# Optimization experiments

Measured on AMD Instinct MI355X. Metric: run time of the kernel, lower is better.

Reference implementation:

```python
import jax, jax.numpy as jnp
import numpy as np

N, E = 50000, 800000
IN_CH, INTER, H1, H2 = 256, 32, 8, 8
C2 = IN_CH // H2  # 32
NEG_SLOPE = 0.2


def setup_inputs() -> dict:
    key = jax.random.key(0)
    ks = jax.random.split(key, 10)
    x = jax.random.normal(ks[0], (N, IN_CH), dtype=jnp.float32)
    edge_index = jax.random.randint(ks[1], (2, E), 0, N, dtype=jnp.int32)
    s = 0.05
    W1 = jax.random.normal(ks[2], (H1 * INTER, IN_CH), dtype=jnp.float32) * s
    att_src1 = jax.random.normal(ks[3], (1, H1, INTER), dtype=jnp.float32) * s
    att_dst1 = jax.random.normal(ks[4], (1, H1, INTER), dtype=jnp.float32) * s
    b1 = jnp.zeros((H1 * INTER,), dtype=jnp.float32)
    W2 = jax.random.normal(ks[5], (H2 * C2, H1 * INTER), dtype=jnp.float32) * s
    att_src2 = jax.random.normal(ks[6], (1, H2, C2), dtype=jnp.float32) * s
    att_dst2 = jax.random.normal(ks[7], (1, H2, C2), dtype=jnp.float32) * s
    b2 = jnp.zeros((H2 * C2,), dtype=jnp.float32)
    return {"x": x, "edge_index": edge_index,
            "W1": W1, "att_src1": att_src1, "att_dst1": att_dst1, "b1": b1,
            "W2": W2, "att_src2": att_src2, "att_dst2": att_dst2, "b2": b2}


def gat_conv(x, edge_index, W, att_src, att_dst, bias, H, C):
    # PyG GATConv (shared lin for src/dst, add_self_loops=False, concat=True)
    n = x.shape[0]
    src, dst = edge_index[0], edge_index[1]
    xw = (x @ W.T).reshape(n, H, C)                     # [N,H,C]
    a_src = jnp.sum(xw * att_src, axis=-1)              # [N,H]
    a_dst = jnp.sum(xw * att_dst, axis=-1)              # [N,H]
    e = a_src[src] + a_dst[dst]                         # [E,H]
    e = jnp.where(e >= 0, e, NEG_SLOPE * e)             # LeakyReLU(0.2)
    # segment softmax over edges grouped by destination node
    m = jax.ops.segment_max(e, dst, num_segments=n)     # [N,H]
    ex = jnp.exp(e - m[dst])
    denom = jax.ops.segment_sum(ex, dst, num_segments=n)
    alpha = ex / (denom[dst] + 1e-16)                   # [E,H]
    # weighted scatter-aggregate of source messages
    msg = xw[src] * alpha[:, :, None]                   # [E,H,C]
    out = jax.ops.segment_sum(msg, dst, num_segments=n) # [N,H,C]
    return out.reshape(n, H * C) + bias


def reference(x, edge_index, W1, att_src1, att_dst1, b1, W2, att_src2, att_dst2, b2):
    h = gat_conv(x, edge_index, W1, att_src1, att_dst1, b1, H1, INTER)
    h = jax.nn.gelu(h, approximate=False)  # F.gelu default is exact
    h = gat_conv(h, edge_index, W2, att_src2, att_dst2, b2, H2, C2)
    return h[-1]  # eval-path super node
```

## Files before the change

### kernel.cpp

```cpp
#include <hip/hip_runtime.h>
#include <math.h>

#define N_NODES 50000
#define N_EDGES 800000
#define TGT     (N_NODES - 1)
#define C2MAX   256
#define KCAP    258
#define ELMAX   256
#define ROWS    (ELMAX + 1)
#define PBLK    8
#define SCANBLK 1024
#define BMWORDS 1568

struct WS {
  int* cnt;
  int* cnt2;
  int* fin_k;
  int* e2src;
  int* g_uniq;
  int* g_slot;
  int* g_misc;
  int* l1src;
  float* W1T4;
  float* W2T4;
  float* g_xw2;
  float* g_as2;
  float* g_ad2;
  float* g_as1;
  float* g_ad1;
  float* g_xw1;
};
__host__ __device__ inline WS carve(char* ws) {
  WS w; int* p = (int*)ws;
  w.cnt = p;    p += 16;
  w.cnt2 = p;   p += 272;
  w.fin_k = p;  p += 272;
  w.e2src = p;  p += C2MAX;
  w.g_uniq = p; p += 272;
  w.g_slot = p; p += C2MAX;
  w.g_misc = p; p += 16;
  w.l1src = p;  p += KCAP * ELMAX;
  float* f = (float*)p;
  w.W1T4 = f;   f += 65536;
  w.W2T4 = f;   f += 65536;
  w.g_xw2 = f;  f += KCAP * 256;
  w.g_as2 = f;  f += KCAP * 8;
  w.g_ad2 = f;  f += KCAP * 8;
  w.g_as1 = f;  f += KCAP * ROWS * 8;
  w.g_ad1 = f;  f += KCAP * ROWS * 8;
  w.g_xw1 = f;
  return w;
}

__global__ __launch_bounds__(256) void k_scan2(const int* __restrict__ eidx,
    const float* __restrict__ W1, const float* __restrict__ W2, char* ws) {
  WS w = carve(ws);
  int t = threadIdx.x;
  __shared__ float lds[64][65];
  if (blockIdx.x < 32) {
    int m  = blockIdx.x >> 4;
    int ti = (blockIdx.x >> 2) & 3, tj = blockIdx.x & 3;
    const float* src = m ? W2 : W1;
    float*       dst = m ? w.W2T4 : w.W1T4;
    int r0 = t >> 6, cc = t & 63;
    float tmp[16];
#pragma unroll
    for (int p = 0; p < 16; ++p)
      tmp[p] = src[(ti * 64 + p * 4 + r0) * 256 + tj * 64 + cc];
#pragma unroll
    for (int p = 0; p < 16; ++p)
      lds[p * 4 + r0][cc] = tmp[p];
    __syncthreads();
    int c40 = t >> 6, o = t & 63;
#pragma unroll
    for (int p2 = 0; p2 < 4; ++p2) {
      int c4l = p2 * 4 + c40;
      float4 v = make_float4(lds[o][4 * c4l + 0], lds[o][4 * c4l + 1],
                             lds[o][4 * c4l + 2], lds[o][4 * c4l + 3]);
      ((float4*)dst)[(tj * 16 + c4l) * 256 + ti * 64 + o] = v;
    }
  }
  int tid = blockIdx.x * 256 + t;
  int nthreads = gridDim.x * 256;
  const int* esrc = eidx;
  const int4* edst4 = (const int4*)(eidx + N_EDGES);
  for (int i = tid; i < N_EDGES / 4; i += nthreads) {
    int4 d = edst4[i];
    int dv[4] = {d.x, d.y, d.z, d.w};
#pragma unroll
    for (int j = 0; j < 4; ++j)
      if (dv[j] == TGT) {
        int p = atomicAdd(&w.cnt[0], 1);
        if (p < C2MAX) w.e2src[p] = esrc[4 * i + j];
      }
  }
}

__global__ __launch_bounds__(256) void k_scan1(const int* __restrict__ eidx, char* ws) {
  WS w = carve(ws);
  int t = threadIdx.x;
  __shared__ int s_e[C2MAX], s_scan[256], s_uniq[KCAP], s_slot[C2MAX], s_kv[2];
  __shared__ unsigned s_bm[BMWORDS];
  int c2 = min(w.cnt[0], C2MAX);
  if (t < c2) s_e[t] = w.e2src[t];
  __syncthreads();
  int firstIdx = t;
  if (t < c2) {
    int s = s_e[t];
    for (int q = 0; q < t; ++q) if (s_e[q] == s) { firstIdx = q; break; }
  }
  s_scan[t] = (t < c2 && firstIdx == t) ? 1 : 0;
  __syncthreads();
  for (int off = 1; off < 256; off <<= 1) {
    int add = (t >= off) ? s_scan[t - off] : 0;
    __syncthreads();
    s_scan[t] += add;
    __syncthreads();
  }
  if (t < c2 && firstIdx == t) s_uniq[s_scan[t] - 1] = s_e[t];
  __syncthreads();
  if (t < c2) s_slot[t] = s_scan[firstIdx] - 1;
  if (t == 0) {
    int K1 = (c2 > 0) ? s_scan[255] : 0;
    int kd = -1;
    for (int i = 0; i < K1; ++i) if (s_uniq[i] == TGT) { kd = i; break; }
    if (kd < 0) { s_uniq[K1] = TGT; kd = K1; K1++; }
    s_kv[0] = K1; s_kv[1] = kd;
  }
  for (int i = t; i < BMWORDS; i += 256) s_bm[i] = 0u;
  __syncthreads();
  int K1 = s_kv[0];
  for (int i = t; i < K1; i += 256) {
    int u = s_uniq[i];
    atomicOr(&s_bm[u >> 5], 1u << (u & 31));
  }
  if (blockIdx.x == 0) {
    for (int i = t; i < K1; i += 256) w.g_uniq[i] = s_uniq[i];
    if (t < c2) w.g_slot[t] = s_slot[t];
    if (t == 0) { w.g_misc[0] = K1; w.g_misc[1] = s_kv[1]; }
  }
  __syncthreads();
  int tid = blockIdx.x * 256 + t;
  int nthreads = gridDim.x * 256;
  const int* esrc = eidx;
  const int4* edst4 = (const int4*)(eidx + N_EDGES);
  for (int i = tid; i < N_EDGES / 4; i += nthreads) {
    int4 d = edst4[i];
    int dv[4] = {d.x, d.y, d.z, d.w};
#pragma unroll
    for (int j = 0; j < 4; ++j) {
      int u = dv[j];
      if ((s_bm[u >> 5] >> (u & 31)) & 1u) {
        int k = 0;
        for (int q = 0; q < K1; ++q) if (s_uniq[q] == u) { k = q; break; }
        int p = atomicAdd(&w.cnt2[k], 1);
        if (p < ELMAX) w.l1src[k * ELMAX + p] = esrc[4 * i + j];
      }
    }
  }
}

__global__ __launch_bounds__(256) void k_fused(const float* __restrict__ x,
    const float* __restrict__ aS1, const float* __restrict__ aD1,
    const float* __restrict__ b1, const float* __restrict__ aS2,
    const float* __restrict__ aD2, const float* __restrict__ b2,
    float* __restrict__ out, char* ws) {
  WS w = carve(ws);
  int K1 = w.g_misc[0];
  int k = blockIdx.x;
  if (k >= K1) return;
  int t = threadIdx.x;
  int ne = min(w.cnt2[k], ELMAX);
  int items = ne + 1;
  int myNode = w.g_uniq[k];
  __shared__ __align__(16) float s_xsT[4 * 256];
  __shared__ float s_redS[4 * 256], s_redD[4 * 256];
  __shared__ float s_as[ROWS * 8];
  __shared__ float s_p[ELMAX * 8];
  __shared__ float s_den[8];
  __shared__ __align__(16) float s_h1[256];
  __shared__ int   s_sl[C2MAX];
  __shared__ int   s_win;
  const float4* W1v = (const float4*)w.W1T4;
  const float4* W2v = (const float4*)w.W2T4;
  const float4* xsT4 = (const float4*)s_xsT;

  for (int b = blockIdx.y; b * 4 < items; b += PBLK) {
    int base = b * 4;
    int na = min(4, items - base);
    int nd[4];
#pragma unroll
    for (int i = 0; i < 4; ++i) {
      int it = base + i;
      nd[i] = (it < ne) ? w.l1src[k * ELMAX + it] : myNode;
    }
#pragma unroll
    for (int i = 0; i < 4; ++i)
      s_xsT[t * 4 + i] = x[(size_t)nd[i] * 256 + t];
    __syncthreads();
    float a0 = 0.f, a1 = 0.f, a2 = 0.f, a3 = 0.f;
    for (int cc = 0; cc < 64; cc += 8) {
      float4 wreg[8];
#pragma unroll
      for (int j = 0; j < 8; ++j)
        wreg[j] = W1v[(size_t)(cc + j) * 256 + t];
#pragma unroll
      for (int j = 0; j < 8; ++j) {
        float4 wv = wreg[j];
        int c4 = cc + j;
        float4 x0 = xsT4[4 * c4 + 0];
        float4 x1 = xsT4[4 * c4 + 1];
        float4 x2 = xsT4[4 * c4 + 2];
        float4 x3 = xsT4[4 * c4 + 3];
        a0 = fmaf(wv.x, x0.x, a0); a0 = fmaf(wv.y, x1.x, a0); a0 = fmaf(wv.z, x2.x, a0); a0 = fmaf(wv.w, x3.x, a0);
        a1 = fmaf(wv.x, x0.y, a1); a1 = fmaf(wv.y, x1.y, a1); a1 = fmaf(wv.z, x2.y, a1); a1 = fmaf(wv.w, x3.y, a1);
        a2 = fmaf(wv.x, x0.z, a2); a2 = fmaf(wv.y, x1.z, a2); a2 = fmaf(wv.z, x2.z, a2); a2 = fmaf(wv.w, x3.z, a2);
        a3 = fmaf(wv.x, x0.w, a3); a3 = fmaf(wv.y, x1.w, a3); a3 = fmaf(wv.z, x2.w, a3); a3 = fmaf(wv.w, x3.w, a3);
      }
    }
    float accs[4] = {a0, a1, a2, a3};
    for (int i = 0; i < na; ++i) {
      int row = k * ROWS + base + i;
      w.g_xw1[(size_t)row * 256 + t] = accs[i];
      s_redS[i * 256 + t] = accs[i] * aS1[t];
      s_redD[i * 256 + t] = accs[i] * aD1[t];
    }
    __syncthreads();
    if (t < 32) {
      int i = t >> 3, h = t & 7;
      if (i < na) {
        float s = 0.f, dd = 0.f;
        for (int q = 0; q < 32; ++q) {
          s  += s_redS[i * 256 + h * 32 + q];
          dd += s_redD[i * 256 + h * 32 + q];
        }
        int row = k * ROWS + base + i;
        w.g_as1[row * 8 + h] = s;
        w.g_ad1[row * 8 + h] = dd;
      }
    }
    __syncthreads();
  }

  __syncthreads();
  if (t == 0) {
    __threadfence();
    int old = __hip_atomic_fetch_add(&w.fin_k[k], 1, __ATOMIC_ACQ_REL, __HIP_MEMORY_SCOPE_AGENT);
    s_win = (old == PBLK - 1);
  }
  __syncthreads();
  if (!s_win) return;
  __threadfence();

  for (int i = t; i < items * 8; i += 256) s_as[i] = w.g_as1[(size_t)(k * ROWS) * 8 + i];
  __syncthreads();
  if (t < 8) {
    int h = t;
    float adst = w.g_ad1[(size_t)(k * ROWS + ne) * 8 + h];
    float m = -INFINITY;
    for (int j = 0; j < ne; ++j) {
      float e = s_as[j * 8 + h] + adst;
      e = (e >= 0.f) ? e : 0.2f * e;
      m = fmaxf(m, e);
    }
    float den = 0.f;
    for (int j = 0; j < ne; ++j) {
      float e = s_as[j * 8 + h] + adst;
      e = (e >= 0.f) ? e : 0.2f * e;
      float p = expf(e - m);
      s_p[j * 8 + h] = p;
      den += p;
    }
    s_den[h] = den + 1e-16f;
  }
  __syncthreads();
  int h = t >> 5;
  float acc = 0.f;
  const float* xwb = w.g_xw1 + (size_t)(k * ROWS) * 256 + t;
  for (int j0 = 0; j0 < ne; j0 += 8) {
    float tmp[8];
#pragma unroll
    for (int j = 0; j < 8; ++j)
      tmp[j] = (j0 + j < ne) ? xwb[(size_t)(j0 + j) * 256] : 0.f;
#pragma unroll
    for (int j = 0; j < 8; ++j)
      if (j0 + j < ne) acc = fmaf(s_p[(j0 + j) * 8 + h], tmp[j], acc);
  }
  float o = (ne > 0) ? acc / s_den[h] : 0.f;
  o += b1[t];
  s_h1[t] = 0.5f * o * (1.f + erff(o * 0.70710678118654752440f));
  __syncthreads();
  float a2s = 0.f;
  const float4* h1v = (const float4*)s_h1;
  for (int cc = 0; cc < 64; cc += 8) {
    float4 wreg[8];
#pragma unroll
    for (int j = 0; j < 8; ++j)
      wreg[j] = W2v[(size_t)(cc + j) * 256 + t];
#pragma unroll
    for (int j = 0; j < 8; ++j) {
      float4 wv = wreg[j];
      float4 hv = h1v[cc + j];
      a2s = fmaf(wv.x, hv.x, a2s); a2s = fmaf(wv.y, hv.y, a2s);
      a2s = fmaf(wv.z, hv.z, a2s); a2s = fmaf(wv.w, hv.w, a2s);
    }
  }
  w.g_xw2[k * 256 + t] = a2s;
  s_redS[t] = a2s * aS2[t];
  s_redD[t] = a2s * aD2[t];
  __syncthreads();
  if (t < 8) {
    float s = 0.f, dd = 0.f;
    for (int q = 0; q < 32; ++q) { s += s_redS[t * 32 + q]; dd += s_redD[t * 32 + q]; }
    w.g_as2[k * 8 + t] = s;
    w.g_ad2[k * 8 + t] = dd;
  }

  __syncthreads();
  if (t == 0) {
    __threadfence();
    int old = __hip_atomic_fetch_add(&w.cnt[1], 1, __ATOMIC_ACQ_REL, __HIP_MEMORY_SCOPE_AGENT);
    s_win = (old == K1 - 1);
  }
  __syncthreads();
  if (!s_win) return;
  __threadfence();

  int c2 = min(w.cnt[0], C2MAX);
  int kd = w.g_misc[1];
  for (int j = t; j < c2; j += 256) s_sl[j] = w.g_slot[j];
  __syncthreads();
  if (t < 8) {
    float adst = w.g_ad2[kd * 8 + t];
    float m = -INFINITY;
    for (int j = 0; j < c2; ++j) {
      float e = w.g_as2[s_sl[j] * 8 + t] + adst;
      e = (e >= 0.f) ? e : 0.2f * e;
      m = fmaxf(m, e);
    }
    float den = 0.f;
    for (int j = 0; j < c2; ++j) {
      float e = w.g_as2[s_sl[j] * 8 + t] + adst;
      e = (e >= 0.f) ? e : 0.2f * e;
      float p = expf(e - m);
      s_p[j * 8 + t] = p;
      den += p;
    }
    s_den[t] = den + 1e-16f;
  }
  __syncthreads();
  float acc2 = 0.f;
  for (int j0 = 0; j0 < c2; j0 += 8) {
    float tmp[8];
#pragma unroll
    for (int j = 0; j < 8; ++j)
      tmp[j] = (j0 + j < c2) ? w.g_xw2[s_sl[j0 + j] * 256 + t] : 0.f;
#pragma unroll
    for (int j = 0; j < 8; ++j)
      if (j0 + j < c2) acc2 = fmaf(s_p[(j0 + j) * 8 + h], tmp[j], acc2);
  }
  float o2 = (c2 > 0) ? acc2 / s_den[h] : 0.f;
  out[t] = o2 + b2[t];
}

extern "C" void kernel_launch(void* const* d_in, const int* in_sizes, int n_in,
                              void* d_out, int out_size, void* d_ws, size_t ws_size,
                              hipStream_t stream) {
  const float* x    = (const float*)d_in[0];
  const int*   eidx = (const int*)d_in[1];
  const float* W1   = (const float*)d_in[2];
  const float* aS1  = (const float*)d_in[3];
  const float* aD1  = (const float*)d_in[4];
  const float* b1   = (const float*)d_in[5];
  const float* W2   = (const float*)d_in[6];
  const float* aS2  = (const float*)d_in[7];
  const float* aD2  = (const float*)d_in[8];
  const float* b2   = (const float*)d_in[9];
  float* out = (float*)d_out;
  char*  ws  = (char*)d_ws;

  hipMemsetAsync(ws, 0, (16 + 272 + 272) * sizeof(int), stream);

  k_scan2<<<SCANBLK, 256, 0, stream>>>(eidx, W1, W2, ws);
  k_scan1<<<SCANBLK, 256, 0, stream>>>(eidx, ws);
  k_fused<<<dim3(KCAP, PBLK), 256, 0, stream>>>(x, aS1, aD1, b1, aS2, aD2, b2, out, ws);
}
```

Baseline: 137.1 us.

## Merge three kernels into one persistent kernel with software grid barriers

```diff
diff --git a/kernel.cpp b/kernel.cpp
--- a/kernel.cpp
+++ b/kernel.cpp
@@ -9,17 +9,13 @@
 #define ELMAX   256
 #define ROWS    (ELMAX + 1)
 #define PBLK    8
-#define SCANBLK 1024
+#define GRID    512
 #define BMWORDS 1568
 
 struct WS {
   int* cnt;
   int* cnt2;
-  int* fin_k;
   int* e2src;
-  int* g_uniq;
-  int* g_slot;
-  int* g_misc;
   int* l1src;
   float* W1T4;
   float* W2T4;
@@ -32,13 +28,9 @@
 };
 __host__ __device__ inline WS carve(char* ws) {
   WS w; int* p = (int*)ws;
-  w.cnt = p;    p += 16;
+  w.cnt = p;    p += 80;
   w.cnt2 = p;   p += 272;
-  w.fin_k = p;  p += 272;
   w.e2src = p;  p += C2MAX;
-  w.g_uniq = p; p += 272;
-  w.g_slot = p; p += C2MAX;
-  w.g_misc = p; p += 16;
   w.l1src = p;  p += KCAP * ELMAX;
   float* f = (float*)p;
   w.W1T4 = f;   f += 65536;
@@ -52,14 +44,44 @@
   return w;
 }
 
-__global__ __launch_bounds__(256) void k_scan2(const int* __restrict__ eidx,
-    const float* __restrict__ W1, const float* __restrict__ W2, char* ws) {
+__device__ inline void gbar(int* c) {
+  __syncthreads();
+  if (threadIdx.x == 0) {
+    __threadfence();
+    __hip_atomic_fetch_add(c, 1, __ATOMIC_ACQ_REL, __HIP_MEMORY_SCOPE_AGENT);
+    int spins = 0;
+    while (__hip_atomic_load(c, __ATOMIC_ACQUIRE, __HIP_MEMORY_SCOPE_AGENT) < GRID) {
+      __builtin_amdgcn_s_sleep(16);
+      if (++spins > (1 << 22)) break;
+    }
+    __threadfence();
+  }
+  __syncthreads();
+}
+
+__global__ __launch_bounds__(256, 2) void k_all(
+    const float* __restrict__ x, const int* __restrict__ eidx,
+    const float* __restrict__ W1, const float* __restrict__ W2,
+    const float* __restrict__ aS1, const float* __restrict__ aD1,
+    const float* __restrict__ b1, const float* __restrict__ aS2,
+    const float* __restrict__ aD2, const float* __restrict__ b2,
+    float* __restrict__ out, char* __restrict__ ws)
+{
   WS w = carve(ws);
-  int t = threadIdx.x;
-  __shared__ float lds[64][65];
-  if (blockIdx.x < 32) {
-    int m  = blockIdx.x >> 4;
-    int ti = (blockIdx.x >> 2) & 3, tj = blockIdx.x & 3;
+  const int t = threadIdx.x;
+  const int blk = blockIdx.x;
+  const int tid = blk * 256 + t;
+  const int nthreads = GRID * 256;
+
+  __shared__ int s_kv[2];
+  __shared__ int s_uniq[KCAP];
+  __shared__ int s_slotp[C2MAX];
+  __shared__ __align__(16) char smem[17664];
+
+  if (blk < 32) {
+    float (*lds)[65] = (float(*)[65])smem;
+    int m  = blk >> 4;
+    int ti = (blk >> 2) & 3, tj = blk & 3;
     const float* src = m ? W2 : W1;
     float*       dst = m ? w.W2T4 : w.W1T4;
     int r0 = t >> 6, cc = t & 63;
@@ -79,288 +101,272 @@
                              lds[o][4 * c4l + 2], lds[o][4 * c4l + 3]);
       ((float4*)dst)[(tj * 16 + c4l) * 256 + ti * 64 + o] = v;
     }
-  }
-  int tid = blockIdx.x * 256 + t;
-  int nthreads = gridDim.x * 256;
-  const int* esrc = eidx;
-  const int4* edst4 = (const int4*)(eidx + N_EDGES);
-  for (int i = tid; i < N_EDGES / 4; i += nthreads) {
-    int4 d = edst4[i];
-    int dv[4] = {d.x, d.y, d.z, d.w};
-#pragma unroll
-    for (int j = 0; j < 4; ++j)
-      if (dv[j] == TGT) {
-        int p = atomicAdd(&w.cnt[0], 1);
-        if (p < C2MAX) w.e2src[p] = esrc[4 * i + j];
-      }
-  }
-}
-
-__global__ __launch_bounds__(256) void k_scan1(const int* __restrict__ eidx, char* ws) {
-  WS w = carve(ws);
-  int t = threadIdx.x;
-  __shared__ int s_e[C2MAX], s_scan[256], s_uniq[KCAP], s_slot[C2MAX], s_kv[2];
-  __shared__ unsigned s_bm[BMWORDS];
-  int c2 = min(w.cnt[0], C2MAX);
-  if (t < c2) s_e[t] = w.e2src[t];
-  __syncthreads();
-  int firstIdx = t;
-  if (t < c2) {
-    int s = s_e[t];
-    for (int q = 0; q < t; ++q) if (s_e[q] == s) { firstIdx = q; break; }
-  }
-  s_scan[t] = (t < c2 && firstIdx == t) ? 1 : 0;
-  __syncthreads();
-  for (int off = 1; off < 256; off <<= 1) {
-    int add = (t >= off) ? s_scan[t - off] : 0;
-    __syncthreads();
-    s_scan[t] += add;
-    __syncthreads();
-  }
-  if (t < c2 && firstIdx == t) s_uniq[s_scan[t] - 1] = s_e[t];
-  __syncthreads();
-  if (t < c2) s_slot[t] = s_scan[firstIdx] - 1;
-  if (t == 0) {
-    int K1 = (c2 > 0) ? s_scan[255] : 0;
-    int kd = -1;
-    for (int i = 0; i < K1; ++i) if (s_uniq[i] == TGT) { kd = i; break; }
-    if (kd < 0) { s_uniq[K1] = TGT; kd = K1; K1++; }
-    s_kv[0] = K1; s_kv[1] = kd;
-  }
-  for (int i = t; i < BMWORDS; i += 256) s_bm[i] = 0u;
-  __syncthreads();
-  int K1 = s_kv[0];
-  for (int i = t; i < K1; i += 256) {
-    int u = s_uniq[i];
-    atomicOr(&s_bm[u >> 5], 1u << (u & 31));
-  }
-  if (blockIdx.x == 0) {
-    for (int i = t; i < K1; i += 256) w.g_uniq[i] = s_uniq[i];
-    if (t < c2) w.g_slot[t] = s_slot[t];
-    if (t == 0) { w.g_misc[0] = K1; w.g_misc[1] = s_kv[1]; }
-  }
-  __syncthreads();
-  int tid = blockIdx.x * 256 + t;
-  int nthreads = gridDim.x * 256;
-  const int* esrc = eidx;
-  const int4* edst4 = (const int4*)(eidx + N_EDGES);
-  for (int i = tid; i < N_EDGES / 4; i += nthreads) {
-    int4 d = edst4[i];
-    int dv[4] = {d.x, d.y, d.z, d.w};
-#pragma unroll
-    for (int j = 0; j < 4; ++j) {
-      int u = dv[j];
-      if ((s_bm[u >> 5] >> (u & 31)) & 1u) {
-        int k = 0;
-        for (int q = 0; q < K1; ++q) if (s_uniq[q] == u) { k = q; break; }
-        int p = atomicAdd(&w.cnt2[k], 1);
-        if (p < ELMAX) w.l1src[k * ELMAX + p] = esrc[4 * i + j];
-      }
-    }
-  }
-}
-
-__global__ __launch_bounds__(256) void k_fused(const float* __restrict__ x,
-    const float* __restrict__ aS1, const float* __restrict__ aD1,
-    const float* __restrict__ b1, const float* __restrict__ aS2,
-    const float* __restrict__ aD2, const float* __restrict__ b2,
-    float* __restrict__ out, char* ws) {
-  WS w = carve(ws);
-  int K1 = w.g_misc[0];
-  int k = blockIdx.x;
-  if (k >= K1) return;
-  int t = threadIdx.x;
-  int ne = min(w.cnt2[k], ELMAX);
-  int items = ne + 1;
-  int myNode = w.g_uniq[k];
-  __shared__ __align__(16) float s_xsT[4 * 256];
-  __shared__ float s_redS[4 * 256], s_redD[4 * 256];
-  __shared__ float s_as[ROWS * 8];
-  __shared__ float s_p[ELMAX * 8];
-  __shared__ float s_den[8];
-  __shared__ __align__(16) float s_h1[256];
-  __shared__ int   s_sl[C2MAX];
-  __shared__ int   s_win;
-  const float4* W1v = (const float4*)w.W1T4;
-  const float4* W2v = (const float4*)w.W2T4;
-  const float4* xsT4 = (const float4*)s_xsT;
-
-  for (int b = blockIdx.y; b * 4 < items; b += PBLK) {
-    int base = b * 4;
-    int na = min(4, items - base);
-    int nd[4];
-#pragma unroll
-    for (int i = 0; i < 4; ++i) {
-      int it = base + i;
-      nd[i] = (it < ne) ? w.l1src[k * ELMAX + it] : myNode;
-    }
-#pragma unroll
-    for (int i = 0; i < 4; ++i)
-      s_xsT[t * 4 + i] = x[(size_t)nd[i] * 256 + t];
-    __syncthreads();
-    float a0 = 0.f, a1 = 0.f, a2 = 0.f, a3 = 0.f;
-    for (int cc = 0; cc < 64; cc += 8) {
-      float4 wreg[8];
+  } else if (blk == 32) {
+    for (int i = t; i < 272; i += 256) w.cnt2[i] = 0;
+  }
+  {
+    const int* esrc = eidx;
+    const int4* edst4 = (const int4*)(eidx + N_EDGES);
+    for (int i = tid; i < N_EDGES / 4; i += nthreads) {
+      int4 d = edst4[i];
+      int dv[4] = {d.x, d.y, d.z, d.w};
+#pragma unroll
+      for (int j = 0; j < 4; ++j)
+        if (dv[j] == TGT) {
+          int p = atomicAdd(&w.cnt[0], 1);
+          if (p < C2MAX) w.e2src[p] = esrc[4 * i + j];
+        }
+    }
+  }
+  gbar(&w.cnt[16]);
+
+  {
+    int* s_e = (int*)smem;
+    int* s_scan = (int*)(smem + 1024);
+    unsigned* s_bm = (unsigned*)(smem + 2048);
+    int c2 = min(w.cnt[0], C2MAX);
+    if (t < c2) s_e[t] = w.e2src[t];
+    __syncthreads();
+    int firstIdx = t;
+    if (t < c2) {
+      int s = s_e[t];
+      for (int q = 0; q < t; ++q) if (s_e[q] == s) { firstIdx = q; break; }
+    }
+    s_scan[t] = (t < c2 && firstIdx == t) ? 1 : 0;
+    __syncthreads();
+    for (int off = 1; off < 256; off <<= 1) {
+      int add = (t >= off) ? s_scan[t - off] : 0;
+      __syncthreads();
+      s_scan[t] += add;
+      __syncthreads();
+    }
+    if (t < c2 && firstIdx == t) s_uniq[s_scan[t] - 1] = s_e[t];
+    __syncthreads();
+    if (blk == 0 && t < c2) s_slotp[t] = s_scan[firstIdx] - 1;
+    if (t == 0) {
+      int K1 = (c2 > 0) ? s_scan[255] : 0;
+      int kd = -1;
+      for (int i = 0; i < K1; ++i) if (s_uniq[i] == TGT) { kd = i; break; }
+      if (kd < 0) { s_uniq[K1] = TGT; kd = K1; K1++; }
+      s_kv[0] = K1; s_kv[1] = kd;
+    }
+    for (int i = t; i < BMWORDS; i += 256) s_bm[i] = 0u;
+    __syncthreads();
+    int K1 = s_kv[0];
+    for (int i = t; i < K1; i += 256) {
+      int u = s_uniq[i];
+      atomicOr(&s_bm[u >> 5], 1u << (u & 31));
+    }
+    __syncthreads();
+    const int* esrc = eidx;
+    const int4* edst4 = (const int4*)(eidx + N_EDGES);
+    for (int i = tid; i < N_EDGES / 4; i += nthreads) {
+      int4 d = edst4[i];
+      int dv[4] = {d.x, d.y, d.z, d.w};
+#pragma unroll
+      for (int j = 0; j < 4; ++j) {
+        int u = dv[j];
+        if ((s_bm[u >> 5] >> (u & 31)) & 1u) {
+          int k = 0;
+          for (int q = 0; q < K1; ++q) if (s_uniq[q] == u) { k = q; break; }
+          int p = atomicAdd(&w.cnt2[k], 1);
+          if (p < ELMAX) w.l1src[k * ELMAX + p] = esrc[4 * i + j];
+        }
+      }
+    }
+  }
+  gbar(&w.cnt[32]);
+
+  {
+    float* s_xsT = (float*)smem;
+    float* s_redS = (float*)(smem + 4096);
+    float* s_redD = (float*)(smem + 8192);
+    const float4* W1v = (const float4*)w.W1T4;
+    const float4* xsT4 = (const float4*)s_xsT;
+    int K1 = s_kv[0];
+    for (int idx = blk; idx < K1 * PBLK; idx += GRID) {
+      int k = idx >> 3, y = idx & 7;
+      int ne = min(w.cnt2[k], ELMAX);
+      int items = ne + 1;
+      int myNode = s_uniq[k];
+      for (int b = y; b * 4 < items; b += PBLK) {
+        int base = b * 4;
+        int na = min(4, items - base);
+        int nd[4];
+#pragma unroll
+        for (int i = 0; i < 4; ++i) {
+          int it = base + i;
+          nd[i] = (it < ne) ? w.l1src[k * ELMAX + it] : myNode;
+        }
+#pragma unroll
+        for (int i = 0; i < 4; ++i)
+          s_xsT[t * 4 + i] = x[(size_t)nd[i] * 256 + t];
+        __syncthreads();
+        float a0 = 0.f, a1 = 0.f, a2 = 0.f, a3 = 0.f;
+        for (int cc = 0; cc < 64; cc += 8) {
+          float4 wreg[8];
+#pragma unroll
+          for (int j = 0; j < 8; ++j)
+            wreg[j] = W1v[(size_t)(cc + j) * 256 + t];
+#pragma unroll
+          for (int j = 0; j < 8; ++j) {
+            float4 wv = wreg[j];
+            int c4 = cc + j;
+            float4 x0 = xsT4[4 * c4 + 0];
+            float4 x1 = xsT4[4 * c4 + 1];
+            float4 x2 = xsT4[4 * c4 + 2];
+            float4 x3 = xsT4[4 * c4 + 3];
+            a0 = fmaf(wv.x, x0.x, a0); a0 = fmaf(wv.y, x1.x, a0); a0 = fmaf(wv.z, x2.x, a0); a0 = fmaf(wv.w, x3.x, a0);
+            a1 = fmaf(wv.x, x0.y, a1); a1 = fmaf(wv.y, x1.y, a1); a1 = fmaf(wv.z, x2.y, a1); a1 = fmaf(wv.w, x3.y, a1);
+            a2 = fmaf(wv.x, x0.z, a2); a2 = fmaf(wv.y, x1.z, a2); a2 = fmaf(wv.z, x2.z, a2); a2 = fmaf(wv.w, x3.z, a2);
+            a3 = fmaf(wv.x, x0.w, a3); a3 = fmaf(wv.y, x1.w, a3); a3 = fmaf(wv.z, x2.w, a3); a3 = fmaf(wv.w, x3.w, a3);
+          }
+        }
+        float accs[4] = {a0, a1, a2, a3};
+        for (int i = 0; i < na; ++i) {
+          int row = k * ROWS + base + i;
+          w.g_xw1[(size_t)row * 256 + t] = accs[i];
+          s_redS[i * 256 + t] = accs[i] * aS1[t];
+          s_redD[i * 256 + t] = accs[i] * aD1[t];
+        }
+        __syncthreads();
+        if (t < 32) {
+          int i = t >> 3, h = t & 7;
+          if (i < na) {
+            float s = 0.f, dd = 0.f;
+            for (int q = 0; q < 32; ++q) {
+              s  += s_redS[i * 256 + h * 32 + q];
+              dd += s_redD[i * 256 + h * 32 + q];
+            }
+            int row = k * ROWS + base + i;
+            w.g_as1[row * 8 + h] = s;
+            w.g_ad1[row * 8 + h] = dd;
+          }
+        }
+        __syncthreads();
+      }
+    }
+  }
+  gbar(&w.cnt[48]);
+
+  {
+    float* s_as = (float*)smem;
+    float* s_p  = (float*)(smem + 8224);
+    float* s_h1 = (float*)(smem + 16416);
+    float* s_den = (float*)(smem + 17440);
+    const float4* W2v = (const float4*)w.W2T4;
+    int K1 = s_kv[0];
+    for (int k = blk; k < K1; k += GRID) {
+      int ne = min(w.cnt2[k], ELMAX);
+      int items = ne + 1;
+      for (int i = t; i < items * 8; i += 256) s_as[i] = w.g_as1[(size_t)(k * ROWS) * 8 + i];
+      __syncthreads();
+      if (t < 8) {
+        int h = t;
+        float adst = w.g_ad1[(size_t)(k * ROWS + ne) * 8 + h];
+        float m = -INFINITY;
+        for (int j = 0; j < ne; ++j) {
+          float e = s_as[j * 8 + h] + adst;
+          e = (e >= 0.f) ? e : 0.2f * e;
+          m = fmaxf(m, e);
+        }
+        float den = 0.f;
+        for (int j = 0; j < ne; ++j) {
+          float e = s_as[j * 8 + h] + adst;
+          e = (e >= 0.f) ? e : 0.2f * e;
+          float pp = expf(e - m);
+          s_p[j * 8 + h] = pp;
+          den += pp;
+        }
+        s_den[h] = den + 1e-16f;
+      }
+      __syncthreads();
+      int h = t >> 5;
+      float acc = 0.f;
+      const float* xwb = w.g_xw1 + (size_t)(k * ROWS) * 256 + t;
+      for (int j0 = 0; j0 < ne; j0 += 8) {
+        float tmp[8];
+#pragma unroll
+        for (int j = 0; j < 8; ++j)
+          tmp[j] = (j0 + j < ne) ? xwb[(size_t)(j0 + j) * 256] : 0.f;
+#pragma unroll
+        for (int j = 0; j < 8; ++j)
+          if (j0 + j < ne) acc = fmaf(s_p[(j0 + j) * 8 + h], tmp[j], acc);
+      }
+      float o = (ne > 0) ? acc / s_den[h] : 0.f;
+      o += b1[t];
+      s_h1[t] = 0.5f * o * (1.f + erff(o * 0.70710678118654752440f));
+      __syncthreads();
+      float a2s = 0.f;
+      const float4* h1v = (const float4*)s_h1;
+      for (int cc = 0; cc < 64; cc += 8) {
+        float4 wreg[8];
+#pragma unroll
+        for (int j = 0; j < 8; ++j)
+          wreg[j] = W2v[(size_t)(cc + j) * 256 + t];
+#pragma unroll
+        for (int j = 0; j < 8; ++j) {
+          float4 wv = wreg[j];
+          float4 hv = h1v[cc + j];
+          a2s = fmaf(wv.x, hv.x, a2s); a2s = fmaf(wv.y, hv.y, a2s);
+          a2s = fmaf(wv.z, hv.z, a2s); a2s = fmaf(wv.w, hv.w, a2s);
+        }
+      }
+      w.g_xw2[k * 256 + t] = a2s;
+      float* rS = s_as;
+      float* rD = s_as + 256;
+      rS[t] = a2s * aS2[t];
+      rD[t] = a2s * aD2[t];
+      __syncthreads();
+      if (t < 8) {
+        float s = 0.f, dd = 0.f;
+        for (int q = 0; q < 32; ++q) { s += rS[t * 32 + q]; dd += rD[t * 32 + q]; }
+        w.g_as2[k * 8 + t] = s;
+        w.g_ad2[k * 8 + t] = dd;
+      }
+      __syncthreads();
+    }
+  }
+  gbar(&w.cnt[64]);
+
+  if (blk == 0) {
+    float* s_p = (float*)smem;
+    float* s_den = (float*)(smem + 8192);
+    int c2 = min(w.cnt[0], C2MAX);
+    int kd = s_kv[1];
+    if (t < 8) {
+      float adst = w.g_ad2[kd * 8 + t];
+      float m = -INFINITY;
+      for (int j = 0; j < c2; ++j) {
+        float e = w.g_as2[s_slotp[j] * 8 + t] + adst;
+        e = (e >= 0.f) ? e : 0.2f * e;
+        m = fmaxf(m, e);
+      }
+      float den = 0.f;
+      for (int j = 0; j < c2; ++j) {
+        float e = w.g_as2[s_slotp[j] * 8 + t] + adst;
+        e = (e >= 0.f) ? e : 0.2f * e;
+        float pp = expf(e - m);
+        s_p[j * 8 + t] = pp;
+        den += pp;
+      }
+      s_den[t] = den + 1e-16f;
+    }
+    __syncthreads();
+    int h = t >> 5;
+    float acc2 = 0.f;
+    for (int j0 = 0; j0 < c2; j0 += 8) {
+      float tmp[8];
 #pragma unroll
       for (int j = 0; j < 8; ++j)
-        wreg[j] = W1v[(size_t)(cc + j) * 256 + t];
-#pragma unroll
-      for (int j = 0; j < 8; ++j) {
-        float4 wv = wreg[j];
-        int c4 = cc + j;
-        float4 x0 = xsT4[4 * c4 + 0];
-        float4 x1 = xsT4[4 * c4 + 1];
-        float4 x2 = xsT4[4 * c4 + 2];
-        float4 x3 = xsT4[4 * c4 + 3];
-        a0 = fmaf(wv.x, x0.x, a0); a0 = fmaf(wv.y, x1.x, a0); a0 = fmaf(wv.z, x2.x, a0); a0 = fmaf(wv.w, x3.x, a0);
-        a1 = fmaf(wv.x, x0.y, a1); a1 = fmaf(wv.y, x1.y, a1); a1 = fmaf(wv.z, x2.y, a1); a1 = fmaf(wv.w, x3.y, a1);
-        a2 = fmaf(wv.x, x0.z, a2); a2 = fmaf(wv.y, x1.z, a2); a2 = fmaf(wv.z, x2.z, a2); a2 = fmaf(wv.w, x3.z, a2);
-        a3 = fmaf(wv.x, x0.w, a3); a3 = fmaf(wv.y, x1.w, a3); a3 = fmaf(wv.z, x2.w, a3); a3 = fmaf(wv.w, x3.w, a3);
-      }
-    }
-    float accs[4] = {a0, a1, a2, a3};
-    for (int i = 0; i < na; ++i) {
-      int row = k * ROWS + base + i;
-      w.g_xw1[(size_t)row * 256 + t] = accs[i];
-      s_redS[i * 256 + t] = accs[i] * aS1[t];
-      s_redD[i * 256 + t] = accs[i] * aD1[t];
-    }
-    __syncthreads();
-    if (t < 32) {
-      int i = t >> 3, h = t & 7;
-      if (i < na) {
-        float s = 0.f, dd = 0.f;
-        for (int q = 0; q < 32; ++q) {
-          s  += s_redS[i * 256 + h * 32 + q];
-          dd += s_redD[i * 256 + h * 32 + q];
-        }
-        int row = k * ROWS + base + i;
-        w.g_as1[row * 8 + h] = s;
-        w.g_ad1[row * 8 + h] = dd;
-      }
-    }
-    __syncthreads();
-  }
-
-  __syncthreads();
-  if (t == 0) {
-    __threadfence();
-    int old = __hip_atomic_fetch_add(&w.fin_k[k], 1, __ATOMIC_ACQ_REL, __HIP_MEMORY_SCOPE_AGENT);
-    s_win = (old == PBLK - 1);
-  }
-  __syncthreads();
-  if (!s_win) return;
-  __threadfence();
-
-  for (int i = t; i < items * 8; i += 256) s_as[i] = w.g_as1[(size_t)(k * ROWS) * 8 + i];
-  __syncthreads();
-  if (t < 8) {
-    int h = t;
-    float adst = w.g_ad1[(size_t)(k * ROWS + ne) * 8 + h];
-    float m = -INFINITY;
-    for (int j = 0; j < ne; ++j) {
-      float e = s_as[j * 8 + h] + adst;
-      e = (e >= 0.f) ? e : 0.2f * e;
-      m = fmaxf(m, e);
-    }
-    float den = 0.f;
-    for (int j = 0; j < ne; ++j) {
-      float e = s_as[j * 8 + h] + adst;
-      e = (e >= 0.f) ? e : 0.2f * e;
-      float p = expf(e - m);
-      s_p[j * 8 + h] = p;
-      den += p;
-    }
-    s_den[h] = den + 1e-16f;
-  }
-  __syncthreads();
-  int h = t >> 5;
-  float acc = 0.f;
-  const float* xwb = w.g_xw1 + (size_t)(k * ROWS) * 256 + t;
-  for (int j0 = 0; j0 < ne; j0 += 8) {
-    float tmp[8];
-#pragma unroll
-    for (int j = 0; j < 8; ++j)
-      tmp[j] = (j0 + j < ne) ? xwb[(size_t)(j0 + j) * 256] : 0.f;
-#pragma unroll
-    for (int j = 0; j < 8; ++j)
-      if (j0 + j < ne) acc = fmaf(s_p[(j0 + j) * 8 + h], tmp[j], acc);
-  }
-  float o = (ne > 0) ? acc / s_den[h] : 0.f;
-  o += b1[t];
-  s_h1[t] = 0.5f * o * (1.f + erff(o * 0.70710678118654752440f));
-  __syncthreads();
-  float a2s = 0.f;
-  const float4* h1v = (const float4*)s_h1;
-  for (int cc = 0; cc < 64; cc += 8) {
-    float4 wreg[8];
-#pragma unroll
-    for (int j = 0; j < 8; ++j)
-      wreg[j] = W2v[(size_t)(cc + j) * 256 + t];
-#pragma unroll
-    for (int j = 0; j < 8; ++j) {
-      float4 wv = wreg[j];
-      float4 hv = h1v[cc + j];
-      a2s = fmaf(wv.x, hv.x, a2s); a2s = fmaf(wv.y, hv.y, a2s);
-      a2s = fmaf(wv.z, hv.z, a2s); a2s = fmaf(wv.w, hv.w, a2s);
-    }
-  }
-  w.g_xw2[k * 256 + t] = a2s;
-  s_redS[t] = a2s * aS2[t];
-  s_redD[t] = a2s * aD2[t];
-  __syncthreads();
-  if (t < 8) {
-    float s = 0.f, dd = 0.f;
-    for (int q = 0; q < 32; ++q) { s += s_redS[t * 32 + q]; dd += s_redD[t * 32 + q]; }
-    w.g_as2[k * 8 + t] = s;
-    w.g_ad2[k * 8 + t] = dd;
-  }
-
-  __syncthreads();
-  if (t == 0) {
-    __threadfence();
-    int old = __hip_atomic_fetch_add(&w.cnt[1], 1, __ATOMIC_ACQ_REL, __HIP_MEMORY_SCOPE_AGENT);
-    s_win = (old == K1 - 1);
-  }
-  __syncthreads();
-  if (!s_win) return;
-  __threadfence();
-
-  int c2 = min(w.cnt[0], C2MAX);
-  int kd = w.g_misc[1];
-  for (int j = t; j < c2; j += 256) s_sl[j] = w.g_slot[j];
-  __syncthreads();
-  if (t < 8) {
-    float adst = w.g_ad2[kd * 8 + t];
-    float m = -INFINITY;
-    for (int j = 0; j < c2; ++j) {
-      float e = w.g_as2[s_sl[j] * 8 + t] + adst;
-      e = (e >= 0.f) ? e : 0.2f * e;
-      m = fmaxf(m, e);
-    }
-    float den = 0.f;
-    for (int j = 0; j < c2; ++j) {
-      float e = w.g_as2[s_sl[j] * 8 + t] + adst;
-      e = (e >= 0.f) ? e : 0.2f * e;
-      float p = expf(e - m);
-      s_p[j * 8 + t] = p;
-      den += p;
-    }
-    s_den[t] = den + 1e-16f;
-  }
-  __syncthreads();
-  float acc2 = 0.f;
-  for (int j0 = 0; j0 < c2; j0 += 8) {
-    float tmp[8];
-#pragma unroll
-    for (int j = 0; j < 8; ++j)
-      tmp[j] = (j0 + j < c2) ? w.g_xw2[s_sl[j0 + j] * 256 + t] : 0.f;
-#pragma unroll
-    for (int j = 0; j < 8; ++j)
-      if (j0 + j < c2) acc2 = fmaf(s_p[(j0 + j) * 8 + h], tmp[j], acc2);
-  }
-  float o2 = (c2 > 0) ? acc2 / s_den[h] : 0.f;
-  out[t] = o2 + b2[t];
+        tmp[j] = (j0 + j < c2) ? w.g_xw2[s_slotp[j0 + j] * 256 + t] : 0.f;
+#pragma unroll
+      for (int j = 0; j < 8; ++j)
+        if (j0 + j < c2) acc2 = fmaf(s_p[(j0 + j) * 8 + h], tmp[j], acc2);
+    }
+    float o2 = (c2 > 0) ? acc2 / s_den[h] : 0.f;
+    out[t] = o2 + b2[t];
+  }
 }
 
 extern "C" void kernel_launch(void* const* d_in, const int* in_sizes, int n_in,
@@ -379,9 +385,8 @@
   float* out = (float*)d_out;
   char*  ws  = (char*)d_ws;
 
-  hipMemsetAsync(ws, 0, (16 + 272 + 272) * sizeof(int), stream);
-
-  k_scan2<<<SCANBLK, 256, 0, stream>>>(eidx, W1, W2, ws);
-  k_scan1<<<SCANBLK, 256, 0, stream>>>(eidx, ws);
-  k_fused<<<dim3(KCAP, PBLK), 256, 0, stream>>>(x, aS1, aD1, b1, aS2, aD2, b2, out, ws);
+  hipMemsetAsync(ws, 0, 80 * sizeof(int), stream);
+
+  k_all<<<dim3(GRID), dim3(256), 0, stream>>>(x, eidx, W1, W2, aS1, aD1, b1,
+                                              aS2, aD2, b2, out, ws);
 }
```

After: 357.1 us. 2.6x slower.

## Split fused GAT kernel into per-node and final kernels, drop atomic handoffs

Applied to the files above, without the earlier changes.

```diff
diff --git a/kernel.cpp b/kernel.cpp
--- a/kernel.cpp
+++ b/kernel.cpp
@@ -8,51 +8,42 @@
 #define KCAP    258
 #define ELMAX   256
 #define ROWS    (ELMAX + 1)
-#define PBLK    8
 #define SCANBLK 1024
 #define BMWORDS 1568
 
 struct WS {
   int* cnt;
   int* cnt2;
-  int* fin_k;
-  int* e2src;
   int* g_uniq;
   int* g_slot;
   int* g_misc;
+  int* e2src;
   int* l1src;
   float* W1T4;
   float* W2T4;
+  float* g_h1;
   float* g_xw2;
-  float* g_as2;
-  float* g_ad2;
-  float* g_as1;
-  float* g_ad1;
   float* g_xw1;
 };
 __host__ __device__ inline WS carve(char* ws) {
   WS w; int* p = (int*)ws;
   w.cnt = p;    p += 16;
   w.cnt2 = p;   p += 272;
-  w.fin_k = p;  p += 272;
-  w.e2src = p;  p += C2MAX;
   w.g_uniq = p; p += 272;
   w.g_slot = p; p += C2MAX;
   w.g_misc = p; p += 16;
+  w.e2src = p;  p += C2MAX;
   w.l1src = p;  p += KCAP * ELMAX;
   float* f = (float*)p;
   w.W1T4 = f;   f += 65536;
   w.W2T4 = f;   f += 65536;
+  w.g_h1 = f;   f += KCAP * 256;
   w.g_xw2 = f;  f += KCAP * 256;
-  w.g_as2 = f;  f += KCAP * 8;
-  w.g_ad2 = f;  f += KCAP * 8;
-  w.g_as1 = f;  f += KCAP * ROWS * 8;
-  w.g_ad1 = f;  f += KCAP * ROWS * 8;
   w.g_xw1 = f;
   return w;
 }
 
-__global__ __launch_bounds__(256) void k_scan2(const int* __restrict__ eidx,
+__global__ __launch_bounds__(256) void k1_prep(const int* __restrict__ eidx,
     const float* __restrict__ W1, const float* __restrict__ W2, char* ws) {
   WS w = carve(ws);
   int t = threadIdx.x;
@@ -96,7 +87,7 @@
   }
 }
 
-__global__ __launch_bounds__(256) void k_scan1(const int* __restrict__ eidx, char* ws) {
+__global__ __launch_bounds__(256) void k2_bucket(const int* __restrict__ eidx, char* ws) {
   WS w = carve(ws);
   int t = threadIdx.x;
   __shared__ int s_e[C2MAX], s_scan[256], s_uniq[KCAP], s_slot[C2MAX], s_kv[2];
@@ -160,33 +151,28 @@
   }
 }
 
-__global__ __launch_bounds__(256) void k_fused(const float* __restrict__ x,
+__global__ __launch_bounds__(256, 2) void k3_dst(const float* __restrict__ x,
     const float* __restrict__ aS1, const float* __restrict__ aD1,
-    const float* __restrict__ b1, const float* __restrict__ aS2,
-    const float* __restrict__ aD2, const float* __restrict__ b2,
-    float* __restrict__ out, char* ws) {
+    const float* __restrict__ b1, char* ws) {
   WS w = carve(ws);
-  int K1 = w.g_misc[0];
-  int k = blockIdx.x;
+  const int t = threadIdx.x;
+  const int k = blockIdx.x;
+  const int K1 = w.g_misc[0];
   if (k >= K1) return;
-  int t = threadIdx.x;
-  int ne = min(w.cnt2[k], ELMAX);
-  int items = ne + 1;
-  int myNode = w.g_uniq[k];
-  __shared__ __align__(16) float s_xsT[4 * 256];
-  __shared__ float s_redS[4 * 256], s_redD[4 * 256];
-  __shared__ float s_as[ROWS * 8];
-  __shared__ float s_p[ELMAX * 8];
-  __shared__ float s_den[8];
-  __shared__ __align__(16) float s_h1[256];
-  __shared__ int   s_sl[C2MAX];
-  __shared__ int   s_win;
+  __shared__ __align__(16) char smem[28800];
   const float4* W1v = (const float4*)w.W1T4;
-  const float4* W2v = (const float4*)w.W2T4;
+  const int ne = min(w.cnt2[k], ELMAX);
+  const int items = ne + 1;
+  const int myNode = w.g_uniq[k];
+
+  float* s_xsT = (float*)smem;
+  float* s_redS = (float*)(smem + 4096);
+  float* s_redD = (float*)(smem + 8192);
+  float* s_as1 = (float*)(smem + 12288);
+  float* s_ad1 = (float*)(smem + 20512);
   const float4* xsT4 = (const float4*)s_xsT;
 
-  for (int b = blockIdx.y; b * 4 < items; b += PBLK) {
-    int base = b * 4;
+  for (int base = 0; base < items; base += 4) {
     int na = min(4, items - base);
     int nd[4];
 #pragma unroll
@@ -220,8 +206,7 @@
     }
     float accs[4] = {a0, a1, a2, a3};
     for (int i = 0; i < na; ++i) {
-      int row = k * ROWS + base + i;
-      w.g_xw1[(size_t)row * 256 + t] = accs[i];
+      w.g_xw1[(size_t)(k * ROWS + base + i) * 256 + t] = accs[i];
       s_redS[i * 256 + t] = accs[i] * aS1[t];
       s_redD[i * 256 + t] = accs[i] * aD1[t];
     }
@@ -234,42 +219,31 @@
           s  += s_redS[i * 256 + h * 32 + q];
           dd += s_redD[i * 256 + h * 32 + q];
         }
-        int row = k * ROWS + base + i;
-        w.g_as1[row * 8 + h] = s;
-        w.g_ad1[row * 8 + h] = dd;
-      }
-    }
-    __syncthreads();
-  }
-
-  __syncthreads();
-  if (t == 0) {
-    __threadfence();
-    int old = __hip_atomic_fetch_add(&w.fin_k[k], 1, __ATOMIC_ACQ_REL, __HIP_MEMORY_SCOPE_AGENT);
-    s_win = (old == PBLK - 1);
-  }
-  __syncthreads();
-  if (!s_win) return;
-  __threadfence();
-
-  for (int i = t; i < items * 8; i += 256) s_as[i] = w.g_as1[(size_t)(k * ROWS) * 8 + i];
-  __syncthreads();
+        s_as1[(base + i) * 8 + h] = s;
+        s_ad1[(base + i) * 8 + h] = dd;
+      }
+    }
+    __syncthreads();
+  }
+
+  float* s_p  = (float*)smem;
+  float* s_den = (float*)(smem + 11264);
   if (t < 8) {
     int h = t;
-    float adst = w.g_ad1[(size_t)(k * ROWS + ne) * 8 + h];
+    float adst = s_ad1[ne * 8 + h];
     float m = -INFINITY;
     for (int j = 0; j < ne; ++j) {
-      float e = s_as[j * 8 + h] + adst;
+      float e = s_as1[j * 8 + h] + adst;
       e = (e >= 0.f) ? e : 0.2f * e;
       m = fmaxf(m, e);
     }
     float den = 0.f;
     for (int j = 0; j < ne; ++j) {
-      float e = s_as[j * 8 + h] + adst;
+      float e = s_as1[j * 8 + h] + adst;
       e = (e >= 0.f) ? e : 0.2f * e;
-      float p = expf(e - m);
-      s_p[j * 8 + h] = p;
-      den += p;
+      float pp = expf(e - m);
+      s_p[j * 8 + h] = pp;
+      den += pp;
     }
     s_den[h] = den + 1e-16f;
   }
@@ -288,73 +262,105 @@
   }
   float o = (ne > 0) ? acc / s_den[h] : 0.f;
   o += b1[t];
-  s_h1[t] = 0.5f * o * (1.f + erff(o * 0.70710678118654752440f));
-  __syncthreads();
-  float a2s = 0.f;
-  const float4* h1v = (const float4*)s_h1;
-  for (int cc = 0; cc < 64; cc += 8) {
-    float4 wreg[8];
-#pragma unroll
-    for (int j = 0; j < 8; ++j)
-      wreg[j] = W2v[(size_t)(cc + j) * 256 + t];
-#pragma unroll
-    for (int j = 0; j < 8; ++j) {
-      float4 wv = wreg[j];
-      float4 hv = h1v[cc + j];
-      a2s = fmaf(wv.x, hv.x, a2s); a2s = fmaf(wv.y, hv.y, a2s);
-      a2s = fmaf(wv.z, hv.z, a2s); a2s = fmaf(wv.w, hv.w, a2s);
-    }
-  }
-  w.g_xw2[k * 256 + t] = a2s;
-  s_redS[t] = a2s * aS2[t];
-  s_redD[t] = a2s * aD2[t];
-  __syncthreads();
+  w.g_h1[k * 256 + t] = 0.5f * o * (1.f + erff(o * 0.70710678118654752440f));
+}
+
+__global__ __launch_bounds__(256, 2) void k4_final(
+    const float* __restrict__ aS2, const float* __restrict__ aD2,
+    const float* __restrict__ b2, float* __restrict__ out, char* ws) {
+  WS w = carve(ws);
+  const int t = threadIdx.x;
+  __shared__ __align__(16) char smem[28800];
+  const float4* W2v = (const float4*)w.W2T4;
+  const int K1 = w.g_misc[0];
+  const int kd = w.g_misc[1];
+  const int c2 = min(w.cnt[0], C2MAX);
+  __shared__ int s_slotp[C2MAX];
+  for (int j = t; j < c2; j += 256) s_slotp[j] = w.g_slot[j];
+
+  float* s_xsT = (float*)smem;
+  float* s_redS = (float*)(smem + 4096);
+  float* s_redD = (float*)(smem + 8192);
+  float* s_as2 = (float*)(smem + 12288);
+  float* s_ad2 = (float*)(smem + 20544);
+  const float4* xsT4 = (const float4*)s_xsT;
+
+  for (int base = 0; base < K1; base += 4) {
+    int na = min(4, K1 - base);
+#pragma unroll
+    for (int i = 0; i < 4; ++i)
+      s_xsT[t * 4 + i] = (base + i < K1) ? w.g_h1[(base + i) * 256 + t] : 0.f;
+    __syncthreads();
+    float a0 = 0.f, a1 = 0.f, a2 = 0.f, a3 = 0.f;
+    for (int cc = 0; cc < 64; cc += 8) {
+      float4 wreg[8];
+#pragma unroll
+      for (int j = 0; j < 8; ++j)
+        wreg[j] = W2v[(size_t)(cc + j) * 256 + t];
+#pragma unroll
+      for (int j = 0; j < 8; ++j) {
+        float4 wv = wreg[j];
+        int c4 = cc + j;
+        float4 x0 = xsT4[4 * c4 + 0];
+        float4 x1 = xsT4[4 * c4 + 1];
+        float4 x2 = xsT4[4 * c4 + 2];
+        float4 x3 = xsT4[4 * c4 + 3];
+        a0 = fmaf(wv.x, x0.x, a0); a0 = fmaf(wv.y, x1.x, a0); a0 = fmaf(wv.z, x2.x, a0); a0 = fmaf(wv.w, x3.x, a0);
+        a1 = fmaf(wv.x, x0.y, a1); a1 = fmaf(wv.y, x1.y, a1); a1 = fmaf(wv.z, x2.y, a1); a1 = fmaf(wv.w, x3.y, a1);
+        a2 = fmaf(wv.x, x0.z, a2); a2 = fmaf(wv.y, x1.z, a2); a2 = fmaf(wv.z, x2.z, a2); a2 = fmaf(wv.w, x3.z, a2);
+        a3 = fmaf(wv.x, x0.w, a3); a3 = fmaf(wv.y, x1.w, a3); a3 = fmaf(wv.z, x2.w, a3); a3 = fmaf(wv.w, x3.w, a3);
+      }
+    }
+    float accs[4] = {a0, a1, a2, a3};
+    for (int i = 0; i < na; ++i) {
+      w.g_xw2[(base + i) * 256 + t] = accs[i];
+      s_redS[i * 256 + t] = accs[i] * aS2[t];
+      s_redD[i * 256 + t] = accs[i] * aD2[t];
+    }
+    __syncthreads();
+    if (t < 32) {
+      int i = t >> 3, h = t & 7;
+      if (i < na) {
+        float s = 0.f, dd = 0.f;
+        for (int q = 0; q < 32; ++q) {
+          s  += s_redS[i * 256 + h * 32 + q];
+          dd += s_redD[i * 256 + h * 32 + q];
+        }
+        s_as2[(base + i) * 8 + h] = s;
+        s_ad2[(base + i) * 8 + h] = dd;
+      }
+    }
+    __syncthreads();
+  }
+
+  float* s_p = (float*)smem;
+  float* s_den = (float*)(smem + 8192);
   if (t < 8) {
-    float s = 0.f, dd = 0.f;
-    for (int q = 0; q < 32; ++q) { s += s_redS[t * 32 + q]; dd += s_redD[t * 32 + q]; }
-    w.g_as2[k * 8 + t] = s;
-    w.g_ad2[k * 8 + t] = dd;
-  }
-
-  __syncthreads();
-  if (t == 0) {
-    __threadfence();
-    int old = __hip_atomic_fetch_add(&w.cnt[1], 1, __ATOMIC_ACQ_REL, __HIP_MEMORY_SCOPE_AGENT);
-    s_win = (old == K1 - 1);
-  }
-  __syncthreads();
-  if (!s_win) return;
-  __threadfence();
-
-  int c2 = min(w.cnt[0], C2MAX);
-  int kd = w.g_misc[1];
-  for (int j = t; j < c2; j += 256) s_sl[j] = w.g_slot[j];
-  __syncthreads();
-  if (t < 8) {
-    float adst = w.g_ad2[kd * 8 + t];
+    float adst = s_ad2[kd * 8 + t];
     float m = -INFINITY;
     for (int j = 0; j < c2; ++j) {
-      float e = w.g_as2[s_sl[j] * 8 + t] + adst;
+      float e = s_as2[s_slotp[j] * 8 + t] + adst;
       e = (e >= 0.f) ? e : 0.2f * e;
       m = fmaxf(m, e);
     }
     float den = 0.f;
     for (int j = 0; j < c2; ++j) {
-      float e = w.g_as2[s_sl[j] * 8 + t] + adst;
+      float e = s_as2[s_slotp[j] * 8 + t] + adst;
       e = (e >= 0.f) ? e : 0.2f * e;
-      float p = expf(e - m);
-      s_p[j * 8 + t] = p;
-      den += p;
+      float pp = expf(e - m);
+      s_p[j * 8 + t] = pp;
+      den += pp;
     }
     s_den[t] = den + 1e-16f;
   }
   __syncthreads();
+  int h = t >> 5;
   float acc2 = 0.f;
   for (int j0 = 0; j0 < c2; j0 += 8) {
     float tmp[8];
 #pragma unroll
     for (int j = 0; j < 8; ++j)
-      tmp[j] = (j0 + j < c2) ? w.g_xw2[s_sl[j0 + j] * 256 + t] : 0.f;
+      tmp[j] = (j0 + j < c2) ? w.g_xw2[s_slotp[j0 + j] * 256 + t] : 0.f;
 #pragma unroll
     for (int j = 0; j < 8; ++j)
       if (j0 + j < c2) acc2 = fmaf(s_p[(j0 + j) * 8 + h], tmp[j], acc2);
@@ -379,9 +385,10 @@
   float* out = (float*)d_out;
   char*  ws  = (char*)d_ws;
 
-  hipMemsetAsync(ws, 0, (16 + 272 + 272) * sizeof(int), stream);
-
-  k_scan2<<<SCANBLK, 256, 0, stream>>>(eidx, W1, W2, ws);
-  k_scan1<<<SCANBLK, 256, 0, stream>>>(eidx, ws);
-  k_fused<<<dim3(KCAP, PBLK), 256, 0, stream>>>(x, aS1, aD1, b1, aS2, aD2, b2, out, ws);
-}
+  hipMemsetAsync(ws, 0, (16 + 272) * sizeof(int), stream);
+
+  k1_prep<<<SCANBLK, 256, 0, stream>>>(eidx, W1, W2, ws);
+  k2_bucket<<<SCANBLK, 256, 0, stream>>>(eidx, ws);
+  k3_dst<<<KCAP, 256, 0, stream>>>(x, aS1, aD1, b1, ws);
+  k4_final<<<1, 256, 0, stream>>>(aS2, aD2, b2, out, ws);
+}
```

New measurement: 189.9 us. +38.5%, slower.
